# Kernel optimization log

Measured on AMD Instinct MI355X. Metric: run time of the kernel, lower is better.

Reference implementation:

```python
import jax, jax.numpy as jnp
import numpy as np

N_NODES = 50000
N_EDGES = 800000
IN_DIM = 128
OUT_DIM = 128
NUM_HEADS = 8
HEAD_DIM = OUT_DIM // NUM_HEADS
LN_EPS = 1e-5


def setup_inputs() -> dict:
    key = jax.random.key(0)
    ks = jax.random.split(key, 8)
    # xavier-uniform bounds
    def xavier(k, shape, fan_in, fan_out):
        a = float(np.sqrt(6.0 / (fan_in + fan_out)))
        return jax.random.uniform(k, shape, jnp.float32, -a, a)
    x = jax.random.normal(ks[0], (N_NODES, IN_DIM), jnp.float32)
    edge_index = jax.random.randint(ks[1], (2, N_EDGES), 0, N_NODES, jnp.int32)
    # store Linear weights as (in, out) so forward is x @ W (same math as torch x @ W.T)
    W_src = xavier(ks[2], (IN_DIM, OUT_DIM), IN_DIM, OUT_DIM)
    W_dst = xavier(ks[3], (IN_DIM, OUT_DIM), IN_DIM, OUT_DIM)
    attn = xavier(ks[4], (NUM_HEADS, HEAD_DIM), HEAD_DIM, NUM_HEADS)
    W_out = xavier(ks[5], (OUT_DIM, OUT_DIM), OUT_DIM, OUT_DIM)
    b_out = jnp.zeros((OUT_DIM,), jnp.float32)
    gamma = jnp.ones((OUT_DIM,), jnp.float32)
    beta = jnp.zeros((OUT_DIM,), jnp.float32)
    return {"x": x, "edge_index": edge_index, "W_src": W_src, "W_dst": W_dst,
            "attn": attn, "W_out": W_out, "b_out": b_out, "gamma": gamma, "beta": beta}


def reference(x, edge_index, W_src, W_dst, attn, W_out, b_out, gamma, beta):
    N = x.shape[0]
    H, D = attn.shape
    src, dst = edge_index[0], edge_index[1]
    # node transforms: (N, H, D)
    h_src = (x @ W_src).reshape(N, H, D)
    h_dst = (x @ W_dst).reshape(N, H, D)
    # per-edge GATv2 attention logits (E, H)
    h_src_e = h_src[src]                                  # (E, H, D)
    e = jax.nn.leaky_relu(h_src_e + h_dst[dst], 0.2)
    s = jnp.einsum('ehd,hd->eh', e, attn)
    # segment (scatter) softmax over incoming edges of each dst node
    m = jax.ops.segment_max(s, dst, num_segments=N)       # (N, H)
    exp = jnp.exp(s - m[dst])
    denom = jax.ops.segment_sum(exp, dst, num_segments=N)
    alpha = exp / (denom[dst] + 1e-8)                     # (E, H)
    # weighted message aggregation
    msg = (h_src_e * alpha[..., None]).reshape(-1, H * D)
    out = jax.ops.segment_sum(msg, dst, num_segments=N)   # (N, H*D)
    out = out @ W_out + b_out
    out = out + x                                          # residual (in_dim == out_dim)
    # LayerNorm
    mu = jnp.mean(out, axis=-1, keepdims=True)
    var = jnp.var(out, axis=-1, keepdims=True)
    out = (out - mu) * jax.lax.rsqrt(var + LN_EPS) * gamma + beta
    return out
```

## Files before the change

kernel.cpp:

```cpp
#include <hip/hip_runtime.h>
#include <hip/hip_bf16.h>

#define HEADS 8
#define CDIM 128
#define CAP 96

typedef __attribute__((ext_vector_type(8))) short bf16x8;
typedef __attribute__((ext_vector_type(4))) float f32x4;

__device__ __forceinline__ unsigned short f2bs(float f) {
    union { __hip_bfloat16 b; unsigned short u; } c;
    c.b = __float2bfloat16(f);
    return c.u;
}

__device__ __forceinline__ float dpp_reduce8(float p) {
    p += __int_as_float(__builtin_amdgcn_update_dpp(0, __float_as_int(p), 0x141, 0xF, 0xF, true));
    p += __int_as_float(__builtin_amdgcn_update_dpp(0, __float_as_int(p), 0xB1,  0xF, 0xF, true));
    p += __int_as_float(__builtin_amdgcn_update_dpp(0, __float_as_int(p), 0x4E,  0xF, 0xF, true));
    return p;
}

__global__ void prep_kernel(const int* __restrict__ ei,
                            int* __restrict__ cnt,
                            int* __restrict__ bucket,
                            const float* __restrict__ Wsrc,
                            const float* __restrict__ Wdst,
                            const float* __restrict__ Wout,
                            unsigned short* __restrict__ WT,
                            unsigned short* __restrict__ WoT, int E4) {
    int i = blockIdx.x * 256 + threadIdx.x;
    if (i < E4) {
        const int4 s4 = ((const int4*)ei)[i];
        const int4 d4 = ((const int4*)(ei))[E4 + i];
        int pos;
        pos = atomicAdd(&cnt[d4.x], 1); if (pos < CAP) bucket[(size_t)d4.x * CAP + pos] = s4.x;
        pos = atomicAdd(&cnt[d4.y], 1); if (pos < CAP) bucket[(size_t)d4.y * CAP + pos] = s4.y;
        pos = atomicAdd(&cnt[d4.z], 1); if (pos < CAP) bucket[(size_t)d4.z * CAP + pos] = s4.z;
        pos = atomicAdd(&cnt[d4.w], 1); if (pos < CAP) bucket[(size_t)d4.w * CAP + pos] = s4.w;
        return;
    }
    i -= E4;
    if (i < 16384)      { WT[i] = f2bs(Wsrc[(i & 127) * CDIM + (i >> 7)]); }
    else if (i < 32768) { int j = i - 16384; WT[16384 + j] = f2bs(Wdst[(j & 127) * CDIM + (j >> 7)]); }
    else if (i < 49152) { int j = i - 32768; WoT[j] = f2bs(Wout[(j & 127) * CDIM + (j >> 7)]); }
}

__global__ __launch_bounds__(256) void transform_mfma64(
        const float* __restrict__ x,
        const unsigned short* __restrict__ WT,
        unsigned short* __restrict__ hsrc,
        unsigned short* __restrict__ hdst, int N) {
    __shared__ unsigned short As[64][136];
    __shared__ unsigned short Bs[128][136];
    const int t = threadIdx.x;
    const int m0 = blockIdx.x * 64;
    const int half = blockIdx.y;
    for (int i = t; i < 64 * 32; i += 256) {
        const int r = i >> 5, kq = i & 31;
        const int gr = m0 + r;
        float4 v = make_float4(0.f, 0.f, 0.f, 0.f);
        if (gr < N) v = *(const float4*)(x + (size_t)gr * CDIM + kq * 4);
        uint2 pk;
        pk.x = (unsigned)f2bs(v.x) | ((unsigned)f2bs(v.y) << 16);
        pk.y = (unsigned)f2bs(v.z) | ((unsigned)f2bs(v.w) << 16);
        *(uint2*)&As[r][kq * 4] = pk;
    }
    const unsigned short* Wb = WT + (size_t)half * 16384;
    for (int i = t; i < 128 * 16; i += 256) {
        const int r = i >> 4, q = i & 15;
        *(uint4*)&Bs[r][q * 8] = *(const uint4*)(Wb + (size_t)r * CDIM + q * 8);
    }
    __syncthreads();
    const int w = t >> 6, lane = t & 63, l16 = lane & 15, quad = lane >> 4;
    const int wm = (w & 1) * 32, wn = (w >> 1) * 64;
    f32x4 acc[2][4];
#pragma unroll
    for (int mi = 0; mi < 2; mi++)
#pragma unroll
        for (int ni = 0; ni < 4; ni++) acc[mi][ni] = (f32x4){0.f, 0.f, 0.f, 0.f};
#pragma unroll
    for (int kc = 0; kc < 4; kc++) {
        const int k0 = kc * 32 + quad * 8;
        bf16x8 af[2], bf[4];
        af[0] = *(const bf16x8*)&As[wm + l16][k0];
        af[1] = *(const bf16x8*)&As[wm + 16 + l16][k0];
#pragma unroll
        for (int ni = 0; ni < 4; ni++)
            bf[ni] = *(const bf16x8*)&Bs[wn + ni * 16 + l16][k0];
#pragma unroll
        for (int mi = 0; mi < 2; mi++)
#pragma unroll
            for (int ni = 0; ni < 4; ni++)
                acc[mi][ni] = __builtin_amdgcn_mfma_f32_16x16x32_bf16(af[mi], bf[ni], acc[mi][ni], 0, 0, 0);
    }
    unsigned short* H = half ? hdst : hsrc;
#pragma unroll
    for (int mi = 0; mi < 2; mi++)
#pragma unroll
        for (int reg = 0; reg < 4; reg++) {
            const int gm = m0 + wm + mi * 16 + quad * 4 + reg;
            if (gm < N) {
#pragma unroll
                for (int ni = 0; ni < 4; ni++)
                    H[(size_t)gm * CDIM + wn + ni * 16 + l16] = f2bs(acc[mi][ni][reg]);
            }
        }
}

__global__ __launch_bounds__(256) void attn_agg4(
        const unsigned short* __restrict__ hsrc,
        const unsigned short* __restrict__ hdst,
        const float* __restrict__ attn,
        const int* __restrict__ cnt,
        const int* __restrict__ bucket,
        unsigned short* __restrict__ aggb) {
    __shared__ int src_lds[4][CAP];
    const int t = threadIdx.x;
    const int w = t >> 6, lane = t & 63;
    const int dst = blockIdx.x * 4 + w;
    int deg = cnt[dst];
    deg = deg > CAP ? CAP : deg;
    for (int j = lane; j < deg; j += 64)
        src_lds[w][j] = bucket[(size_t)dst * CAP + j];

    const unsigned hu = *(const unsigned*)(hdst + (size_t)dst * CDIM + lane * 2);
    const float hd0 = __uint_as_float(hu << 16);
    const float hd1 = __uint_as_float(hu & 0xffff0000u);
    const float2 a2 = ((const float2*)attn)[lane];
    const unsigned short* hb = hsrc + lane * 2;

    float l = 0.f, acc0 = 0.f, acc1 = 0.f;
    for (int j0 = 0; j0 < deg; j0 += 8) {
        unsigned vv[8];
#pragma unroll
        for (int p = 0; p < 8; p++) {
            const int j = j0 + p;
            vv[p] = (j < deg) ? *(const unsigned*)(hb + (size_t)src_lds[w][j] * CDIM) : 0u;
        }
#pragma unroll
        for (int p = 0; p < 8; p++) {
            const int j = j0 + p;
            if (j < deg) {
                const float v0 = __uint_as_float(vv[p] << 16);
                const float v1 = __uint_as_float(vv[p] & 0xffff0000u);
                float e0 = v0 + hd0; e0 = fmaxf(e0, 0.2f * e0);
                float e1 = v1 + hd1; e1 = fmaxf(e1, 0.2f * e1);
                const float pp = dpp_reduce8(e0 * a2.x + e1 * a2.y);
                const float wgt = __expf(pp);
                l += wgt;
                acc0 = fmaf(wgt, v0, acc0);
                acc1 = fmaf(wgt, v1, acc1);
            }
        }
    }
    const float r = 1.f / (l + 1e-8f);
    const unsigned o = (unsigned)f2bs(acc0 * r) | ((unsigned)f2bs(acc1 * r) << 16);
    *(unsigned*)(aggb + (size_t)dst * CDIM + lane * 2) = o;
}

__global__ __launch_bounds__(256) void out_mfma_ln64(
        const unsigned short* __restrict__ aggb,
        const float* __restrict__ x,
        const unsigned short* __restrict__ WoT,
        const float* __restrict__ bo,
        const float* __restrict__ gam,
        const float* __restrict__ bet,
        float* __restrict__ out, int N) {
    __shared__ unsigned short As[64][136];
    __shared__ unsigned short Bs[128][136];
    __shared__ float red1[64][2], red2[64][2];
    __shared__ float s_mu[64], s_rs[64];
    const int t = threadIdx.x;
    const int m0 = blockIdx.x * 64;
    for (int i = t; i < 64 * 16; i += 256) {
        const int r = i >> 4, q = i & 15;
        const int gr = m0 + r;
        uint4 v = make_uint4(0u, 0u, 0u, 0u);
        if (gr < N) v = *(const uint4*)(aggb + (size_t)gr * CDIM + q * 8);
        *(uint4*)&As[r][q * 8] = v;
    }
    for (int i = t; i < 128 * 16; i += 256) {
        const int r = i >> 4, q = i & 15;
        *(uint4*)&Bs[r][q * 8] = *(const uint4*)(WoT + (size_t)r * CDIM + q * 8);
    }
    __syncthreads();
    const int w = t >> 6, lane = t & 63, l16 = lane & 15, quad = lane >> 4;
    const int wm = (w & 1) * 32, wn = (w >> 1) * 64;
    f32x4 acc[2][4];
#pragma unroll
    for (int mi = 0; mi < 2; mi++)
#pragma unroll
        for (int ni = 0; ni < 4; ni++) acc[mi][ni] = (f32x4){0.f, 0.f, 0.f, 0.f};
#pragma unroll
    for (int kc = 0; kc < 4; kc++) {
        const int k0 = kc * 32 + quad * 8;
        bf16x8 af[2], bf[4];
        af[0] = *(const bf16x8*)&As[l16 + wm][k0];
        af[1] = *(const bf16x8*)&As[l16 + wm + 16][k0];
#pragma unroll
        for (int ni = 0; ni < 4; ni++)
            bf[ni] = *(const bf16x8*)&Bs[wn + ni * 16 + l16][k0];
#pragma unroll
        for (int mi = 0; mi < 2; mi++)
#pragma unroll
            for (int ni = 0; ni < 4; ni++)
                acc[mi][ni] = __builtin_amdgcn_mfma_f32_16x16x32_bf16(af[mi], bf[ni], acc[mi][ni], 0, 0, 0);
    }
    float bi[4], g4[4], be4[4];
#pragma unroll
    for (int ni = 0; ni < 4; ni++) {
        const int n = wn + ni * 16 + l16;
        bi[ni] = bo[n]; g4[ni] = gam[n]; be4[ni] = bet[n];
    }
#pragma unroll
    for (int mi = 0; mi < 2; mi++)
#pragma unroll
        for (int reg = 0; reg < 4; reg++) {
            const int gm = m0 + wm + mi * 16 + quad * 4 + reg;
#pragma unroll
            for (int ni = 0; ni < 4; ni++) {
                const float xr = (gm < N) ? x[(size_t)gm * CDIM + wn + ni * 16 + l16] : 0.f;
                acc[mi][ni][reg] += bi[ni] + xr;
            }
        }
#pragma unroll
    for (int mi = 0; mi < 2; mi++)
#pragma unroll
        for (int reg = 0; reg < 4; reg++) {
            float s1 = acc[mi][0][reg] + acc[mi][1][reg] + acc[mi][2][reg] + acc[mi][3][reg];
            float s2 = acc[mi][0][reg] * acc[mi][0][reg] + acc[mi][1][reg] * acc[mi][1][reg]
                     + acc[mi][2][reg] * acc[mi][2][reg] + acc[mi][3][reg] * acc[mi][3][reg];
            s1 += __shfl_xor(s1, 1, 16); s1 += __shfl_xor(s1, 2, 16);
            s1 += __shfl_xor(s1, 4, 16); s1 += __shfl_xor(s1, 8, 16);
            s2 += __shfl_xor(s2, 1, 16); s2 += __shfl_xor(s2, 2, 16);
            s2 += __shfl_xor(s2, 4, 16); s2 += __shfl_xor(s2, 8, 16);
            if (l16 == 0) {
                const int row = wm + mi * 16 + quad * 4 + reg;
                red1[row][w >> 1] = s1;
                red2[row][w >> 1] = s2;
            }
        }
    __syncthreads();
    if (t < 64) {
        const float s1 = red1[t][0] + red1[t][1];
        const float s2 = red2[t][0] + red2[t][1];
        const float mu = s1 * (1.f / 128.f);
        const float var = s2 * (1.f / 128.f) - mu * mu;
        s_mu[t] = mu;
        s_rs[t] = rsqrtf(var + 1e-5f);
    }
    __syncthreads();
#pragma unroll
    for (int mi = 0; mi < 2; mi++)
#pragma unroll
        for (int reg = 0; reg < 4; reg++) {
            const int row = wm + mi * 16 + quad * 4 + reg;
            const int gm = m0 + row;
            if (gm < N) {
                const float mu = s_mu[row], rs = s_rs[row];
#pragma unroll
                for (int ni = 0; ni < 4; ni++)
                    out[(size_t)gm * CDIM + wn + ni * 16 + l16] =
                        (acc[mi][ni][reg] - mu) * rs * g4[ni] + be4[ni];
            }
        }
}

extern "C" void kernel_launch(void* const* d_in, const int* in_sizes, int n_in,
                              void* d_out, int out_size, void* d_ws, size_t ws_size,
                              hipStream_t stream) {
    const float* x    = (const float*)d_in[0];
    const int*   ei   = (const int*)d_in[1];
    const float* Wsrc = (const float*)d_in[2];
    const float* Wdst = (const float*)d_in[3];
    const float* attn = (const float*)d_in[4];
    const float* Wout = (const float*)d_in[5];
    const float* bo   = (const float*)d_in[6];
    const float* gam  = (const float*)d_in[7];
    const float* bet  = (const float*)d_in[8];
    float* out = (float*)d_out;

    const int N = in_sizes[0] / CDIM;
    const int E = in_sizes[1] / 2;
    const int NX = N * CDIM;

    unsigned short* hsrc_b = (unsigned short*)d_ws;
    unsigned short* hdst_b = hsrc_b + (size_t)NX;
    unsigned short* aggb   = hdst_b + (size_t)NX;
    unsigned short* WT     = aggb + (size_t)NX;
    unsigned short* WoT    = WT + 32768;
    int* cnt    = (int*)(WoT + 16384);
    int* bucket = cnt + N;

    hipMemsetAsync(cnt, 0, (size_t)N * sizeof(int), stream);

    const int E4 = E / 4;
    const int prep_total = E4 + 49152;
    prep_kernel<<<(prep_total + 255) / 256, 256, 0, stream>>>(ei, cnt, bucket, Wsrc, Wdst, Wout, WT, WoT, E4);
    transform_mfma64<<<dim3((N + 63) / 64, 2), 256, 0, stream>>>(x, WT, hsrc_b, hdst_b, N);
    attn_agg4<<<N / 4, 256, 0, stream>>>(hsrc_b, hdst_b, attn, cnt, bucket, aggb);
    out_mfma_ln64<<<(N + 63) / 64, 256, 0, stream>>>(aggb, x, WoT, bo, gam, bet, out, N);
}
```

Measured before the change: 211.2 us.

## Shard edge bucketing by destination per block and deepen gather unroll

The prep kernel now splits edges into chunks of 2048 handled by 8 blocks each, and each block only inserts edges whose destination falls in its shard (dst mod 8). This likely aims to keep the atomic counters and bucket writes for a destination on one XCD's L2, relying on round-robin block placement. The cost is that every block re-reads the chunk's destination indices. Separately, the attention aggregation unroll grows from 8 to 16 outstanding gathers to improve memory-level parallelism, at the cost of more registers.

```diff
diff --git a/kernel.cpp b/kernel.cpp
--- a/kernel.cpp
+++ b/kernel.cpp
@@ -4,6 +4,7 @@
 #define HEADS 8
 #define CDIM 128
 #define CAP 96
+#define CHUNK 2048
 
 typedef __attribute__((ext_vector_type(8))) short bf16x8;
 typedef __attribute__((ext_vector_type(4))) float f32x4;
@@ -21,26 +22,31 @@
     return p;
 }
 
-__global__ void prep_kernel(const int* __restrict__ ei,
-                            int* __restrict__ cnt,
-                            int* __restrict__ bucket,
-                            const float* __restrict__ Wsrc,
-                            const float* __restrict__ Wdst,
-                            const float* __restrict__ Wout,
-                            unsigned short* __restrict__ WT,
-                            unsigned short* __restrict__ WoT, int E4) {
-    int i = blockIdx.x * 256 + threadIdx.x;
-    if (i < E4) {
-        const int4 s4 = ((const int4*)ei)[i];
-        const int4 d4 = ((const int4*)(ei))[E4 + i];
-        int pos;
-        pos = atomicAdd(&cnt[d4.x], 1); if (pos < CAP) bucket[(size_t)d4.x * CAP + pos] = s4.x;
-        pos = atomicAdd(&cnt[d4.y], 1); if (pos < CAP) bucket[(size_t)d4.y * CAP + pos] = s4.y;
-        pos = atomicAdd(&cnt[d4.z], 1); if (pos < CAP) bucket[(size_t)d4.z * CAP + pos] = s4.z;
-        pos = atomicAdd(&cnt[d4.w], 1); if (pos < CAP) bucket[(size_t)d4.w * CAP + pos] = s4.w;
+__global__ __launch_bounds__(256) void prep_kernel(
+        const int* __restrict__ ei,
+        int* __restrict__ cnt,
+        int* __restrict__ bucket,
+        const float* __restrict__ Wsrc,
+        const float* __restrict__ Wdst,
+        const float* __restrict__ Wout,
+        unsigned short* __restrict__ WT,
+        unsigned short* __restrict__ WoT, int E, int nedgeblk) {
+    const int b = blockIdx.x;
+    if (b < nedgeblk) {
+        const int shard = b & 7;
+        const int base = (b >> 3) * CHUNK;
+        int end = base + CHUNK; if (end > E) end = E;
+        for (int e = base + (int)threadIdx.x; e < end; e += 256) {
+            const int dst = ei[E + e];
+            if ((dst & 7) == shard) {
+                const int src = ei[e];
+                const int pos = atomicAdd(&cnt[dst], 1);
+                if (pos < CAP) bucket[(size_t)dst * CAP + pos] = src;
+            }
+        }
         return;
     }
-    i -= E4;
+    int i = (b - nedgeblk) * 256 + threadIdx.x;
     if (i < 16384)      { WT[i] = f2bs(Wsrc[(i & 127) * CDIM + (i >> 7)]); }
     else if (i < 32768) { int j = i - 16384; WT[16384 + j] = f2bs(Wdst[(j & 127) * CDIM + (j >> 7)]); }
     else if (i < 49152) { int j = i - 32768; WoT[j] = f2bs(Wout[(j & 127) * CDIM + (j >> 7)]); }
@@ -108,7 +114,7 @@
         }
 }
 
-__global__ __launch_bounds__(256) void attn_agg4(
+__global__ __launch_bounds__(256) void attn_agg5(
         const unsigned short* __restrict__ hsrc,
         const unsigned short* __restrict__ hdst,
         const float* __restrict__ attn,
@@ -131,15 +137,15 @@
     const unsigned short* hb = hsrc + lane * 2;
 
     float l = 0.f, acc0 = 0.f, acc1 = 0.f;
-    for (int j0 = 0; j0 < deg; j0 += 8) {
-        unsigned vv[8];
-#pragma unroll
-        for (int p = 0; p < 8; p++) {
+    for (int j0 = 0; j0 < deg; j0 += 16) {
+        unsigned vv[16];
+#pragma unroll
+        for (int p = 0; p < 16; p++) {
             const int j = j0 + p;
             vv[p] = (j < deg) ? *(const unsigned*)(hb + (size_t)src_lds[w][j] * CDIM) : 0u;
         }
 #pragma unroll
-        for (int p = 0; p < 8; p++) {
+        for (int p = 0; p < 16; p++) {
             const int j = j0 + p;
             if (j < deg) {
                 const float v0 = __uint_as_float(vv[p] << 16);
@@ -295,10 +301,11 @@
 
     hipMemsetAsync(cnt, 0, (size_t)N * sizeof(int), stream);
 
-    const int E4 = E / 4;
-    const int prep_total = E4 + 49152;
-    prep_kernel<<<(prep_total + 255) / 256, 256, 0, stream>>>(ei, cnt, bucket, Wsrc, Wdst, Wout, WT, WoT, E4);
+    const int ngroups  = (E + CHUNK - 1) / CHUNK;
+    const int nedgeblk = ngroups * 8;
+    const int nwblk    = 49152 / 256;
+    prep_kernel<<<nedgeblk + nwblk, 256, 0, stream>>>(ei, cnt, bucket, Wsrc, Wdst, Wout, WT, WoT, E, nedgeblk);
     transform_mfma64<<<dim3((N + 63) / 64, 2), 256, 0, stream>>>(x, WT, hsrc_b, hdst_b, N);
-    attn_agg4<<<N / 4, 256, 0, stream>>>(hsrc_b, hdst_b, attn, cnt, bucket, aggb);
+    attn_agg5<<<N / 4, 256, 0, stream>>>(hsrc_b, hdst_b, attn, cnt, bucket, aggb);
     out_mfma_ln64<<<(N + 63) / 64, 256, 0, stream>>>(aggb, x, WoT, bo, gam, bet, out, N);
 }
```

After: 201.7 us. 1.05x faster.
